# Optimization experiments

Hardware: AMD Instinct MI355X
Metric: run time of the kernel (lower is better)

The kernel has to match this reference:

```python
import jax, jax.numpy as jnp
import numpy as np

WIDTHS = [2, 3, 5, 8, 13, 21, 34, 55, 89, 26]  # ragged one-hot feature widths, sum = 256
NSEG = len(WIDTHS)
B, IN = 8192, 256
LAYOUT = [1024, 1024, 1024, 256]
EPS = 1e-5  # BatchNorm1d default eps
TAU = 1.0


def setup_inputs() -> dict:
    key = jax.random.key(0)
    ks = iter(jax.random.split(key, 64))
    inp = {"x": jax.random.normal(next(ks), (B, IN), jnp.float32)}
    prev = IN
    for i, fc in enumerate(LAYOUT):
        inp[f"W{i}"] = jax.random.normal(next(ks), (fc, prev), jnp.float32) / np.float32(np.sqrt(prev))
        inp[f"b{i}"] = 0.01 * jax.random.normal(next(ks), (fc,), jnp.float32)
        if i + 1 < len(LAYOUT):  # Residual blocks carry BatchNorm params (eval mode)
            inp[f"g{i}"] = 1.0 + 0.1 * jax.random.normal(next(ks), (fc,), jnp.float32)
            inp[f"be{i}"] = 0.1 * jax.random.normal(next(ks), (fc,), jnp.float32)
            inp[f"rm{i}"] = 0.1 * jax.random.normal(next(ks), (fc,), jnp.float32)
            inp[f"rv{i}"] = 0.75 + 0.5 * jax.random.uniform(next(ks), (fc,), dtype=jnp.float32)
        prev += fc
    inp["seg_ids"] = jnp.asarray(np.repeat(np.arange(NSEG), WIDTHS), jnp.int32)  # [256]
    return inp


def _residual(x, W, b, g, be, rm, rv):
    # Linear -> eval-mode BatchNorm1d -> ReLU -> concat([out, input])
    h = x @ W.T + b
    h = (h - rm) * (g * jax.lax.rsqrt(rv + EPS)) + be
    return jnp.concatenate([jax.nn.relu(h), x], axis=1)


def _segment_softmax(x, seg_ids):
    # Fused segmented softmax over ragged feature groups (replaces per-feature Python loop)
    xt = x.T / TAU                                            # [F, B]
    m = jax.ops.segment_max(xt, seg_ids, num_segments=NSEG)   # [NSEG, B]
    e = jnp.exp(xt - m[seg_ids])
    s = jax.ops.segment_sum(e, seg_ids, num_segments=NSEG)
    return (e / s[seg_ids]).T                                 # [B, F]


def reference(x, W0, b0, g0, be0, rm0, rv0, W1, b1, g1, be1, rm1, rv1,
              W2, b2, g2, be2, rm2, rv2, W3, b3, seg_ids):
    h = _residual(x, W0, b0, g0, be0, rm0, rv0)   # [B, 1280]
    h = _residual(h, W1, b1, g1, be1, rm1, rv1)   # [B, 2304]
    h = _residual(h, W2, b2, g2, be2, rm2, rv2)   # [B, 3328]
    h = h @ W3.T + b3                              # [B, 256]
    return _segment_softmax(h, seg_ids)
```

## Files before the change

kernel.cpp:

```cpp
#include <hip/hip_runtime.h>
#include <hip/hip_fp16.h>


#define LDH 3328
#define NROWS 8192

typedef _Float16 f16x8 __attribute__((ext_vector_type(8)));
typedef _Float16 f16x4 __attribute__((ext_vector_type(4)));
typedef float f32x4 __attribute__((ext_vector_type(4)));

__constant__ int c_bnd[11] = {0, 2, 5, 10, 18, 31, 52, 86, 141, 230, 256};

__device__ __forceinline__ void async_cp16(const _Float16* g, _Float16* l) {
  __builtin_amdgcn_global_load_lds(
      (__attribute__((address_space(1))) void*)g,
      (__attribute__((address_space(3))) void*)l, 16, 0, 0);
}

__device__ __forceinline__ _Float16 f2h(float f) { return (_Float16)f; }

__global__ void prep_kernel(const float* __restrict__ s0,
                            const float* __restrict__ s1,
                            const float* __restrict__ s2,
                            const float* __restrict__ s3,
                            const float* __restrict__ x,
                            const float* __restrict__ b3,
                            _Float16* __restrict__ d0,
                            _Float16* __restrict__ d1,
                            _Float16* __restrict__ d2,
                            _Float16* __restrict__ d3,
                            _Float16* __restrict__ H, float* __restrict__ out,
                            int n0, int n1, int n2, int n3, int n4, int n5) {
  int i = blockIdx.x * blockDim.x + threadIdx.x;
  if (i >= n5) return;
  if (i >= n4) {
    const int j = i - n4;
    const int c = (j & 63) * 4;
    *(float4*)&out[(size_t)j * 4] = *(const float4*)&b3[c];
    return;
  }
  if (i >= n3) {
    const int j = i - n3;
    const int row = j >> 6;
    const int c = (j & 63) * 4;
    const float4 v = *(const float4*)&x[(size_t)j * 4];
    f16x4 h = {f2h(v.x), f2h(v.y), f2h(v.z), f2h(v.w)};
    *(f16x4*)&H[(size_t)row * LDH + 3072 + c] = h;
    return;
  }
  const float* s;
  _Float16* d;
  if (i < n0) {
    s = s0; d = d0;
  } else if (i < n1) {
    s = s1 - (size_t)n0 * 4; d = d1 - (size_t)n0 * 4;
  } else if (i < n2) {
    s = s2 - (size_t)n1 * 4; d = d2 - (size_t)n1 * 4;
  } else {
    s = s3 - (size_t)n2 * 4; d = d3 - (size_t)n2 * 4;
  }
  const float4 v = *(const float4*)&s[(size_t)i * 4];
  f16x4 h = {f2h(v.x), f2h(v.y), f2h(v.z), f2h(v.w)};
  *(f16x4*)&d[(size_t)i * 4] = h;
}


#define BUFSZ 24576
#define ABOFF 16384

#define STA(Ab, q, k0)                                                       \
  async_cp16(A + (size_t)(row0 + (q) * 64 + srow) * LDH + (k0) + sgc,        \
             (Ab) + ((q) * 64 + wave * 8) * 64)
#define STB(Bb, h, k0)                                                       \
  async_cp16(W + (size_t)(col0 + (h) * 64 + srow) * K + (k0) + sgc,          \
             (Bb) + ((h) * 64 + wave * 8) * 64)

#define LOADQ(QM, QN)                                                        \
  {                                                                          \
    const int ra0 = wr * 64 + (QM) * 32 + fr;                                \
    const int ra1 = ra0 + 16;                                                \
    const int rb0 = wc * 64 + (QN) * 32 + fr;                                \
    const int rb1 = rb0 + 16;                                                \
    av[0][0] = *(const f16x8*)&Ac[ra0 * 64 + ((q2 ^ (ra0 & 7)) * 8)];        \
    av[0][1] = *(const f16x8*)&Ac[ra0 * 64 + (((q2 + 4) ^ (ra0 & 7)) * 8)];  \
    av[1][0] = *(const f16x8*)&Ac[ra1 * 64 + ((q2 ^ (ra1 & 7)) * 8)];        \
    av[1][1] = *(const f16x8*)&Ac[ra1 * 64 + (((q2 + 4) ^ (ra1 & 7)) * 8)];  \
    bv[0][0] = *(const f16x8*)&Bc[rb0 * 64 + ((q2 ^ (rb0 & 7)) * 8)];        \
    bv[0][1] = *(const f16x8*)&Bc[rb0 * 64 + (((q2 + 4) ^ (rb0 & 7)) * 8)];  \
    bv[1][0] = *(const f16x8*)&Bc[rb1 * 64 + ((q2 ^ (rb1 & 7)) * 8)];        \
    bv[1][1] = *(const f16x8*)&Bc[rb1 * 64 + (((q2 + 4) ^ (rb1 & 7)) * 8)];  \
  }

#define MF(a, b, c) __builtin_amdgcn_mfma_f32_16x16x32_f16(a, b, c, 0, 0, 0)

#define MFMAQ(QM, QN)                                                         \
  __builtin_amdgcn_s_setprio(1);                                              \
  acc[(QM)*2+0][(QN)*2+0] = MF(av[0][0], bv[0][0], acc[(QM)*2+0][(QN)*2+0]);  \
  acc[(QM)*2+0][(QN)*2+1] = MF(av[0][0], bv[1][0], acc[(QM)*2+0][(QN)*2+1]);  \
  acc[(QM)*2+1][(QN)*2+0] = MF(av[1][0], bv[0][0], acc[(QM)*2+1][(QN)*2+0]);  \
  acc[(QM)*2+1][(QN)*2+1] = MF(av[1][0], bv[1][0], acc[(QM)*2+1][(QN)*2+1]);  \
  acc[(QM)*2+0][(QN)*2+0] = MF(av[0][1], bv[0][1], acc[(QM)*2+0][(QN)*2+0]);  \
  acc[(QM)*2+0][(QN)*2+1] = MF(av[0][1], bv[1][1], acc[(QM)*2+0][(QN)*2+1]);  \
  acc[(QM)*2+1][(QN)*2+0] = MF(av[1][1], bv[0][1], acc[(QM)*2+1][(QN)*2+0]);  \
  acc[(QM)*2+1][(QN)*2+1] = MF(av[1][1], bv[1][1], acc[(QM)*2+1][(QN)*2+1]);  \
  __builtin_amdgcn_s_setprio(0);

#define GITER(VMSTR, ISS, k0n)                                               \
  {                                                                          \
    _Float16* Ac = lds_ + cur * BUFSZ;                                       \
    _Float16* Bc = Ac + ABOFF;                                               \
    _Float16* An = lds_ + nxt * BUFSZ;                                       \
    _Float16* Bn = An + ABOFF;                                               \
    f16x8 av[2][2], bv[2][2];                                                \
    if (ISS) { STA(An, 0, k0n); STA(An, 1, k0n); }                           \
    asm volatile("s_waitcnt " VMSTR ::: "memory");                           \
    __builtin_amdgcn_s_barrier();                                            \
    LOADQ(0, 0);                                                             \
    MFMAQ(0, 0);                                                             \
    __builtin_amdgcn_s_barrier();                                            \
    if (ISS) { STA(An, 2, k0n); STA(An, 3, k0n); }                           \
    LOADQ(0, 1);                                                             \
    __builtin_amdgcn_s_barrier();                                            \
    MFMAQ(0, 1);                                                             \
    __builtin_amdgcn_s_barrier();                                            \
    if (ISS) { STB(Bn, 0, k0n); }                                            \
    LOADQ(1, 0);                                                             \
    __builtin_amdgcn_s_barrier();                                            \
    MFMAQ(1, 0);                                                             \
    __builtin_amdgcn_s_barrier();                                            \
    if (ISS) { STB(Bn, 1, k0n); }                                            \
    LOADQ(1, 1);                                                             \
    __builtin_amdgcn_s_barrier();                                            \
    MFMAQ(1, 1);                                                             \
    __builtin_amdgcn_s_barrier();                                            \
  }

__device__ __forceinline__ void gemm_loop(const _Float16* __restrict__ A,
                                          const _Float16* __restrict__ W,
                                          int K, int kbase, int nt, int row0,
                                          int col0, int tid, _Float16* lds_,
                                          f32x4 (&acc)[4][4]) {
  const int lane = tid & 63;
  const int wave = tid >> 6;
  const int wr = wave >> 1;
  const int wc = wave & 1;
  const int fr = lane & 15;
  const int q2 = lane >> 4;
  const int srow = tid >> 3;
  const int sgc = ((tid & 7) ^ (srow & 7)) * 8;

  {
    _Float16* A0 = lds_;
    _Float16* B0 = lds_ + ABOFF;
    STA(A0, 0, kbase); STA(A0, 1, kbase); STA(A0, 2, kbase); STA(A0, 3, kbase);
    STB(B0, 0, kbase); STB(B0, 1, kbase);
    _Float16* A1 = lds_ + BUFSZ;
    _Float16* B1 = A1 + ABOFF;
    STA(A1, 0, kbase + 64); STA(A1, 1, kbase + 64);
    STA(A1, 2, kbase + 64); STA(A1, 3, kbase + 64);
    STB(B1, 0, kbase + 64); STB(B1, 1, kbase + 64);
  }

  int cur = 0, nxt = 2;
  int t = 0;
  for (; t + 2 < nt; ++t) {
    const int k0n = kbase + (t + 2) * 64;
    GITER("vmcnt(8)", 1, k0n);
    cur = cur == 2 ? 0 : cur + 1;
    nxt = nxt == 2 ? 0 : nxt + 1;
  }
  {
    const int k0n = 0;
    GITER("vmcnt(6)", 0, k0n);
    cur = cur == 2 ? 0 : cur + 1;
    GITER("vmcnt(0)", 0, k0n);
  }
}

__launch_bounds__(512, 2) __global__
void gemm_bn_8ph(const _Float16* __restrict__ A, int K,
                 const _Float16* __restrict__ W,
                 const float* __restrict__ bias,
                 const float* __restrict__ g, const float* __restrict__ be,
                 const float* __restrict__ rm, const float* __restrict__ rv,
                 _Float16* __restrict__ outH, int outOff) {
  extern __shared__ _Float16 lds_[];
  const int tid = threadIdx.x;
  const int lane = tid & 63;
  const int wave = tid >> 6;
  const int wr = wave >> 1;
  const int wc = wave & 1;
  const int fr = lane & 15;
  const int q2 = lane >> 4;
  const int row0 = blockIdx.x * 256;
  const int col0 = blockIdx.y * 128;

  f32x4 acc[4][4] = {};
  gemm_loop(A, W, K, 0, K >> 6, row0, col0, tid, lds_, acc);

#pragma unroll
  for (int tn = 0; tn < 4; ++tn) {
    const int n = col0 + wc * 64 + tn * 16 + fr;
    const float alpha = g[n] * rsqrtf(rv[n] + 1e-5f);
    const float beta = (bias[n] - rm[n]) * alpha + be[n];
#pragma unroll
    for (int tm = 0; tm < 4; ++tm) {
      const int rbase = row0 + wr * 64 + tm * 16 + q2 * 4;
#pragma unroll
      for (int r = 0; r < 4; ++r) {
        float v = acc[tm][tn][r] * alpha + beta;
        v = fmaxf(v, 0.0f);
        outH[(size_t)(rbase + r) * LDH + outOff + n] = f2h(v);
      }
    }
  }
}

__launch_bounds__(512, 2) __global__
void gemm_out_8ph(const _Float16* __restrict__ A,
                  const _Float16* __restrict__ W, float* __restrict__ out) {
  extern __shared__ _Float16 lds_[];
  const int tid = threadIdx.x;
  const int lane = tid & 63;
  const int wave = tid >> 6;
  const int wr = wave >> 1;
  const int wc = wave & 1;
  const int fr = lane & 15;
  const int q2 = lane >> 4;
  const int row0 = blockIdx.x * 256;
  const int cb = blockIdx.y & 1;
  const int ks = blockIdx.y >> 1;
  const int col0 = cb * 128;
  const int K = 3328;

  f32x4 acc[4][4] = {};
  gemm_loop(A, W, K, ks * 832, 13, row0, col0, tid, lds_, acc);

#pragma unroll
  for (int tn = 0; tn < 4; ++tn) {
    const int n = col0 + wc * 64 + tn * 16 + fr;
#pragma unroll
    for (int tm = 0; tm < 4; ++tm) {
      const int rbase = row0 + wr * 64 + tm * 16 + q2 * 4;
#pragma unroll
      for (int r = 0; r < 4; ++r)
        atomicAdd(&out[(size_t)(rbase + r) * 256 + n], acc[tm][tn][r]);
    }
  }
}

__global__ void segsoftmax_kernel(float* __restrict__ out,
                                  const int* __restrict__ segids) {
  __shared__ float vals[4][256];
  __shared__ float red[4][10];
  const int w = threadIdx.x >> 6;
  const int l = threadIdx.x & 63;
  const int row = blockIdx.x * 4 + w;
  float4 v = *(float4*)&out[(size_t)row * 256 + l * 4];
  *(float4*)&vals[w][l * 4] = v;
  __syncthreads();
  if (l < 10) {
    float m = -1e30f;
    for (int j = c_bnd[l]; j < c_bnd[l + 1]; ++j) m = fmaxf(m, vals[w][j]);
    red[w][l] = m;
  }
  __syncthreads();
  const int4 s4 = *(const int4*)&segids[l * 4];
  float4 e;
  e.x = expf(v.x - red[w][s4.x]);
  e.y = expf(v.y - red[w][s4.y]);
  e.z = expf(v.z - red[w][s4.z]);
  e.w = expf(v.w - red[w][s4.w]);
  *(float4*)&vals[w][l * 4] = e;
  __syncthreads();
  if (l < 10) {
    float s = 0.0f;
    for (int j = c_bnd[l]; j < c_bnd[l + 1]; ++j) s += vals[w][j];
    red[w][l] = s;
  }
  __syncthreads();
  float4 o;
  o.x = e.x / red[w][s4.x];
  o.y = e.y / red[w][s4.y];
  o.z = e.z / red[w][s4.z];
  o.w = e.w / red[w][s4.w];
  *(float4*)&out[(size_t)row * 256 + l * 4] = o;
}

extern "C" void kernel_launch(void* const* d_in, const int* in_sizes, int n_in,
                              void* d_out, int out_size, void* d_ws,
                              size_t ws_size, hipStream_t stream) {
  const float* x = (const float*)d_in[0];
  const float* W0 = (const float*)d_in[1];
  const float* b0 = (const float*)d_in[2];
  const float* g0 = (const float*)d_in[3];
  const float* be0 = (const float*)d_in[4];
  const float* rm0 = (const float*)d_in[5];
  const float* rv0 = (const float*)d_in[6];
  const float* W1 = (const float*)d_in[7];
  const float* b1 = (const float*)d_in[8];
  const float* g1 = (const float*)d_in[9];
  const float* be1 = (const float*)d_in[10];
  const float* rm1 = (const float*)d_in[11];
  const float* rv1 = (const float*)d_in[12];
  const float* W2 = (const float*)d_in[13];
  const float* b2 = (const float*)d_in[14];
  const float* g2 = (const float*)d_in[15];
  const float* be2 = (const float*)d_in[16];
  const float* rm2 = (const float*)d_in[17];
  const float* rv2 = (const float*)d_in[18];
  const float* W3 = (const float*)d_in[19];
  const float* b3 = (const float*)d_in[20];
  const int* seg = (const int*)d_in[21];
  float* out = (float*)d_out;

  _Float16* H = (_Float16*)d_ws;
  size_t off = (size_t)NROWS * LDH;
  _Float16* Wh0 = H + off; off += 1024 * 256;
  _Float16* Wh1 = H + off; off += 1024 * 1280;
  _Float16* Wh2 = H + off; off += 1024 * 2304;
  _Float16* Wh3 = H + off;

  static bool attr_done = false;
  if (!attr_done) {
    hipFuncSetAttribute(reinterpret_cast<const void*>(gemm_bn_8ph),
                        hipFuncAttributeMaxDynamicSharedMemorySize, 147456);
    hipFuncSetAttribute(reinterpret_cast<const void*>(gemm_out_8ph),
                        hipFuncAttributeMaxDynamicSharedMemorySize, 147456);
    attr_done = true;
  }

  const int n0 = 65536, n1 = n0 + 327680, n2 = n1 + 589824, n3 = n2 + 212992;
  const int n4 = n3 + 524288, n5 = n4 + 524288;
  prep_kernel<<<(n5 + 255) / 256, 256, 0, stream>>>(
      W0, W1, W2, W3, x, b3, Wh0, Wh1, Wh2, Wh3, H, out, n0, n1, n2, n3, n4,
      n5);

  gemm_bn_8ph<<<dim3(32, 8), 512, 147456, stream>>>(
      H + 3072, 256, Wh0, b0, g0, be0, rm0, rv0, H, 2048);
  gemm_bn_8ph<<<dim3(32, 8), 512, 147456, stream>>>(
      H + 2048, 1280, Wh1, b1, g1, be1, rm1, rv1, H, 1024);
  gemm_bn_8ph<<<dim3(32, 8), 512, 147456, stream>>>(
      H + 1024, 2304, Wh2, b2, g2, be2, rm2, rv2, H, 0);
  gemm_out_8ph<<<dim3(32, 8), 512, 147456, stream>>>(H, Wh3, out);
  segsoftmax_kernel<<<2048, 256, 0, stream>>>(out, seg);
}
```

Measured before the change: 256.6 us.

## Restructure GEMM main loop into two k-halves with fewer barriers

Replaces the eight-phase quadrant schedule (four LDS-load/MFMA phases with a barrier around each) with two k-half phases per tile. Each phase loads all four A and B fragments for that half and issues a 4x4 MFMA block. The global-to-LDS prefetch is split across the two halves, and vmcnt waits are re-tuned to match. Launch bounds drop from 2 to 1 blocks per CU, which allows more registers for the larger fragment set but may reduce occupancy and latency hiding.

```diff
diff --git a/kernel.cpp b/kernel.cpp
--- a/kernel.cpp
+++ b/kernel.cpp
@@ -75,64 +75,49 @@
   async_cp16(W + (size_t)(col0 + (h) * 64 + srow) * K + (k0) + sgc,          \
              (Bb) + ((h) * 64 + wave * 8) * 64)
 
-#define LOADQ(QM, QN)                                                        \
-  {                                                                          \
-    const int ra0 = wr * 64 + (QM) * 32 + fr;                                \
-    const int ra1 = ra0 + 16;                                                \
-    const int rb0 = wc * 64 + (QN) * 32 + fr;                                \
-    const int rb1 = rb0 + 16;                                                \
-    av[0][0] = *(const f16x8*)&Ac[ra0 * 64 + ((q2 ^ (ra0 & 7)) * 8)];        \
-    av[0][1] = *(const f16x8*)&Ac[ra0 * 64 + (((q2 + 4) ^ (ra0 & 7)) * 8)];  \
-    av[1][0] = *(const f16x8*)&Ac[ra1 * 64 + ((q2 ^ (ra1 & 7)) * 8)];        \
-    av[1][1] = *(const f16x8*)&Ac[ra1 * 64 + (((q2 + 4) ^ (ra1 & 7)) * 8)];  \
-    bv[0][0] = *(const f16x8*)&Bc[rb0 * 64 + ((q2 ^ (rb0 & 7)) * 8)];        \
-    bv[0][1] = *(const f16x8*)&Bc[rb0 * 64 + (((q2 + 4) ^ (rb0 & 7)) * 8)];  \
-    bv[1][0] = *(const f16x8*)&Bc[rb1 * 64 + ((q2 ^ (rb1 & 7)) * 8)];        \
-    bv[1][1] = *(const f16x8*)&Bc[rb1 * 64 + (((q2 + 4) ^ (rb1 & 7)) * 8)];  \
+#define LOADK(KQ)                                                             \
+  {                                                                           \
+    _Pragma("unroll") for (int t = 0; t < 4; ++t) {                           \
+      const int ra = wr * 64 + t * 16 + fr;                                   \
+      av[t] =                                                                 \
+          *(const f16x8*)&Ac[ra * 64 + (((q2 + 4 * (KQ)) ^ (ra & 7)) * 8)];   \
+      const int rb = wc * 64 + t * 16 + fr;                                   \
+      bv[t] =                                                                 \
+          *(const f16x8*)&Bc[rb * 64 + (((q2 + 4 * (KQ)) ^ (rb & 7)) * 8)];   \
+    }                                                                         \
   }
 
 #define MF(a, b, c) __builtin_amdgcn_mfma_f32_16x16x32_f16(a, b, c, 0, 0, 0)
 
-#define MFMAQ(QM, QN)                                                         \
+#define MFMAK()                                                               \
   __builtin_amdgcn_s_setprio(1);                                              \
-  acc[(QM)*2+0][(QN)*2+0] = MF(av[0][0], bv[0][0], acc[(QM)*2+0][(QN)*2+0]);  \
-  acc[(QM)*2+0][(QN)*2+1] = MF(av[0][0], bv[1][0], acc[(QM)*2+0][(QN)*2+1]);  \
-  acc[(QM)*2+1][(QN)*2+0] = MF(av[1][0], bv[0][0], acc[(QM)*2+1][(QN)*2+0]);  \
-  acc[(QM)*2+1][(QN)*2+1] = MF(av[1][0], bv[1][0], acc[(QM)*2+1][(QN)*2+1]);  \
-  acc[(QM)*2+0][(QN)*2+0] = MF(av[0][1], bv[0][1], acc[(QM)*2+0][(QN)*2+0]);  \
-  acc[(QM)*2+0][(QN)*2+1] = MF(av[0][1], bv[1][1], acc[(QM)*2+0][(QN)*2+1]);  \
-  acc[(QM)*2+1][(QN)*2+0] = MF(av[1][1], bv[0][1], acc[(QM)*2+1][(QN)*2+0]);  \
-  acc[(QM)*2+1][(QN)*2+1] = MF(av[1][1], bv[1][1], acc[(QM)*2+1][(QN)*2+1]);  \
+  _Pragma("unroll") for (int tm = 0; tm < 4; ++tm)                            \
+      _Pragma("unroll") for (int tn = 0; tn < 4; ++tn) acc[tm][tn] =          \
+          MF(av[tm], bv[tn], acc[tm][tn]);                                    \
   __builtin_amdgcn_s_setprio(0);
 
-#define GITER(VMSTR, ISS, k0n)                                               \
-  {                                                                          \
-    _Float16* Ac = lds_ + cur * BUFSZ;                                       \
-    _Float16* Bc = Ac + ABOFF;                                               \
-    _Float16* An = lds_ + nxt * BUFSZ;                                       \
-    _Float16* Bn = An + ABOFF;                                               \
-    f16x8 av[2][2], bv[2][2];                                                \
-    if (ISS) { STA(An, 0, k0n); STA(An, 1, k0n); }                           \
-    asm volatile("s_waitcnt " VMSTR ::: "memory");                           \
-    __builtin_amdgcn_s_barrier();                                            \
-    LOADQ(0, 0);                                                             \
-    MFMAQ(0, 0);                                                             \
-    __builtin_amdgcn_s_barrier();                                            \
-    if (ISS) { STA(An, 2, k0n); STA(An, 3, k0n); }                           \
-    LOADQ(0, 1);                                                             \
-    __builtin_amdgcn_s_barrier();                                            \
-    MFMAQ(0, 1);                                                             \
-    __builtin_amdgcn_s_barrier();                                            \
-    if (ISS) { STB(Bn, 0, k0n); }                                            \
-    LOADQ(1, 0);                                                             \
-    __builtin_amdgcn_s_barrier();                                            \
-    MFMAQ(1, 0);                                                             \
-    __builtin_amdgcn_s_barrier();                                            \
-    if (ISS) { STB(Bn, 1, k0n); }                                            \
-    LOADQ(1, 1);                                                             \
-    __builtin_amdgcn_s_barrier();                                            \
-    MFMAQ(1, 1);                                                             \
-    __builtin_amdgcn_s_barrier();                                            \
+#define GITER2(STG, VM, k0n)                                                  \
+  {                                                                           \
+    _Float16* Ac = lds_ + cur * BUFSZ;                                        \
+    _Float16* Bc = Ac + ABOFF;                                                \
+    _Float16* An = lds_ + nxt * BUFSZ;                                        \
+    _Float16* Bn = An + ABOFF;                                                \
+    f16x8 av[4], bv[4];                                                       \
+                \
+    LOADK(0);                                                                 \
+    if (STG) { STA(An, 0, k0n); STA(An, 1, k0n); STB(Bn, 0, k0n); }           \
+    __builtin_amdgcn_s_barrier();                                             \
+    asm volatile("s_waitcnt lgkmcnt(0)" ::: "memory");                        \
+    MFMAK();                                                                  \
+    __builtin_amdgcn_s_barrier();                                             \
+                                                                 \
+    LOADK(1);                                                                 \
+    if (STG) { STA(An, 2, k0n); STA(An, 3, k0n); STB(Bn, 1, k0n); }           \
+    asm volatile("s_waitcnt " VM ::: "memory");                               \
+    __builtin_amdgcn_s_barrier();                                             \
+    asm volatile("s_waitcnt lgkmcnt(0)" ::: "memory");                        \
+    MFMAK();                                                                  \
+    __builtin_amdgcn_s_barrier();                                             \
   }
 
 __device__ __forceinline__ void gemm_loop(const _Float16* __restrict__ A,
@@ -159,25 +144,22 @@
     STA(A1, 0, kbase + 64); STA(A1, 1, kbase + 64);
     STA(A1, 2, kbase + 64); STA(A1, 3, kbase + 64);
     STB(B1, 0, kbase + 64); STB(B1, 1, kbase + 64);
+    asm volatile("s_waitcnt vmcnt(6)" ::: "memory");
+    __builtin_amdgcn_s_barrier();
   }
 
   int cur = 0, nxt = 2;
-  int t = 0;
-  for (; t + 2 < nt; ++t) {
-    const int k0n = kbase + (t + 2) * 64;
-    GITER("vmcnt(8)", 1, k0n);
+  for (int t = 0; t + 2 < nt; ++t) {
+    GITER2(1, "vmcnt(6)", kbase + (t + 2) * 64);
     cur = cur == 2 ? 0 : cur + 1;
     nxt = nxt == 2 ? 0 : nxt + 1;
   }
-  {
-    const int k0n = 0;
-    GITER("vmcnt(6)", 0, k0n);
-    cur = cur == 2 ? 0 : cur + 1;
-    GITER("vmcnt(0)", 0, k0n);
-  }
-}
-
-__launch_bounds__(512, 2) __global__
+  GITER2(0, "vmcnt(0)", 0);
+  cur = cur == 2 ? 0 : cur + 1;
+  GITER2(0, "vmcnt(0)", 0);
+}
+
+__launch_bounds__(512, 1) __global__
 void gemm_bn_8ph(const _Float16* __restrict__ A, int K,
                  const _Float16* __restrict__ W,
                  const float* __restrict__ bias,
@@ -216,7 +198,7 @@
   }
 }
 
-__launch_bounds__(512, 2) __global__
+__launch_bounds__(512, 1) __global__
 void gemm_out_8ph(const _Float16* __restrict__ A,
                   const _Float16* __restrict__ W, float* __restrict__ out) {
   extern __shared__ _Float16 lds_[];
```

After: 245.9 us. -4.1%, faster.
